# Optimization experiments

Hardware: AMD Instinct MI355X
Metric: run time of the kernel (lower is better)

Reference implementation:

```python
import jax, jax.numpy as jnp
import numpy as np

PAD = 0.1
RESO = 128           # plane_resolution
HID = 128            # hidden_dim
CDIM = 128           # c_dim
NBLK = 5             # n_blocks
PLANES = (('xz', (0, 2)), ('xy', (0, 1)), ('yz', (1, 2)))


def normalize_coordinate(p, dims):
    # p: (B,T,3) -> (B,T,2) in [0, 1)
    xy = p[..., list(dims)] / (1.0 + PAD + 1e-3) + 0.5
    return jnp.clip(xy, 0.0, 1.0 - 1e-5)


def coordinate2index(xy, reso):
    g = (xy * reso).astype(jnp.int32)          # (B,T,2)
    return g[..., 0] + reso * g[..., 1]        # (B,T) flat cell index


def scatter_max_gather(vals, idx, n_cells):
    # vals: (B,T,F), idx: (B,T) -> per-cell max gathered back to points (B,T,F)
    B, T, F = vals.shape
    flat_idx = (idx + jnp.arange(B, dtype=idx.dtype)[:, None] * n_cells).reshape(-1)
    fea = jax.ops.segment_max(vals.reshape(B * T, F), flat_idx, num_segments=B * n_cells)
    return fea[flat_idx].reshape(B, T, F)


def scatter_mean_plane(c, idx, n_cells):
    # c: (B,T,C), idx: (B,T) -> (B, n_cells, C); empty cells stay 0
    B, T, C = c.shape
    flat_idx = (idx + jnp.arange(B, dtype=idx.dtype)[:, None] * n_cells).reshape(-1)
    s = jax.ops.segment_sum(c.reshape(B * T, C), flat_idx, num_segments=B * n_cells)
    cnt = jax.ops.segment_sum(jnp.ones((B * T,), c.dtype), flat_idx, num_segments=B * n_cells)
    return (s / jnp.maximum(cnt, 1.0)[:, None]).reshape(B, n_cells, C)


def resnet_block(x, W0, b0, W1, b1, Ws):
    # ResnetBlockFC(2H -> H), size_h = H, shortcut = Linear(no bias)
    net = jax.nn.relu(x) @ W0 + b0
    dx = jax.nn.relu(net) @ W1 + b1
    return x @ Ws + dx


def setup_inputs() -> dict:
    key = jax.random.key(0)
    ks = jax.random.split(key, 10)
    B, T = 2, 32768
    s = 0.05
    return {
        'p': jax.random.uniform(ks[0], (B, T, 3), jnp.float32, -0.5, 0.5),
        'fc_pos_W': s * jax.random.normal(ks[1], (3, 2 * HID), jnp.float32),
        'fc_pos_b': s * jax.random.normal(ks[2], (2 * HID,), jnp.float32),
        'blocks_W0': s * jax.random.normal(ks[3], (NBLK, 2 * HID, HID), jnp.float32),
        'blocks_b0': s * jax.random.normal(ks[4], (NBLK, HID), jnp.float32),
        'blocks_W1': s * jax.random.normal(ks[5], (NBLK, HID, HID), jnp.float32),
        'blocks_b1': s * jax.random.normal(ks[6], (NBLK, HID), jnp.float32),
        'blocks_Ws': s * jax.random.normal(ks[7], (NBLK, 2 * HID, HID), jnp.float32),
        'fc_c_W': s * jax.random.normal(ks[8], (HID, CDIM), jnp.float32),
        'fc_c_b': s * jax.random.normal(ks[9], (CDIM,), jnp.float32),
    }


def reference(p, fc_pos_W, fc_pos_b, blocks_W0, blocks_b0, blocks_W1, blocks_b1,
              blocks_Ws, fc_c_W, fc_c_b):
    B, T, _ = p.shape
    R2 = RESO * RESO
    index = {k: coordinate2index(normalize_coordinate(p, d), RESO) for k, d in PLANES}

    net = p @ fc_pos_W + fc_pos_b                       # (B,T,2H)
    net = resnet_block(net, blocks_W0[0], blocks_b0[0],
                       blocks_W1[0], blocks_b1[0], blocks_Ws[0])  # (B,T,H)
    for i in range(1, NBLK):
        pooled = sum(scatter_max_gather(net, index[k], R2) for k, _ in PLANES)
        net = jnp.concatenate([net, pooled], axis=-1)   # (B,T,2H)
        net = resnet_block(net, blocks_W0[i], blocks_b0[i],
                           blocks_W1[i], blocks_b1[i], blocks_Ws[i])

    c = net @ fc_c_W + fc_c_b                           # (B,T,C)
    planes = []
    for k, _ in PLANES:  # order: xz, xy, yz
        fea = scatter_mean_plane(c, index[k], R2)       # (B,R2,C)
        planes.append(fea.transpose(0, 2, 1).reshape(B, CDIM, RESO, RESO))
    return jnp.stack(planes)                            # (3,B,C,R,R)
```

## Files before the change

### kernel.cpp

```cpp
#include <hip/hip_runtime.h>

#define TT 65536
#define R2 16384

typedef _Float16 f16x8 __attribute__((ext_vector_type(8)));
typedef float    f32x4 __attribute__((ext_vector_type(4)));
typedef unsigned u32x4 __attribute__((ext_vector_type(4)));

#define MFMA16 __builtin_amdgcn_mfma_f32_16x16x32_f16

__device__ __forceinline__ unsigned short f2h(float f){
    _Float16 h = (_Float16)f;
    return __builtin_bit_cast(unsigned short, h);
}
__device__ __forceinline__ float h2f(unsigned short u){
    return (float)__builtin_bit_cast(_Float16, u);
}
__device__ __forceinline__ unsigned relu2(unsigned w){
    unsigned s = w & 0x80008000u;
    unsigned mask = ((s >> 15) * 0x7FFFu) | s;
    return w & ~mask;
}
__device__ __forceinline__ float nrm(float a){
    float v = a / 1.101f + 0.5f;
    v = fmaxf(v, 0.0f);
    v = fminf(v, 0.99999f);
    return v;
}

__global__ __launch_bounds__(256) void k_repack(const float* __restrict__ W0,
        const float* __restrict__ W1, const float* __restrict__ Ws,
        const float* __restrict__ Wc, unsigned short* __restrict__ out){
    int e = blockIdx.x*256 + threadIdx.x;
    const float* src; int r;
    if (e < 409600){
        int i = e / 81920; r = e % 81920;
        if (r < 32768)      { src = W0 + (size_t)i*32768; }
        else if (r < 49152) { src = W1 + (size_t)i*16384; r -= 32768; }
        else                { src = Ws + (size_t)i*32768; r -= 49152; }
    } else { src = Wc; r = e - 409600; }
    int j = r & 7, l = (r >> 3) & 63, t = (r >> 9) & 7, ks = r >> 12;
    int k = ks*32 + (l >> 4)*8 + j;
    int n = t*16 + (l & 15);
    out[e] = f2h(src[k*128 + n]);
}

__global__ __launch_bounds__(256) void k_idxhist(const float* __restrict__ p,
        int* __restrict__ idx, int* __restrict__ cnt){
    int pt = blockIdx.x*256 + threadIdx.x;
    float p0 = p[pt*3+0], p1 = p[pt*3+1], p2 = p[pt*3+2];
    int g0 = (int)(nrm(p0)*128.f);
    int g1 = (int)(nrm(p1)*128.f);
    int g2 = (int)(nrm(p2)*128.f);
    int i0 = g0 + 128*g2, i1 = g0 + 128*g1, i2 = g1 + 128*g2;
    idx[0*TT + pt] = i0;
    idx[1*TT + pt] = i1;
    idx[2*TT + pt] = i2;
    int b14 = (pt >> 15) << 14;
    atomicAdd(&cnt[0*32768 + b14 + i0], 1);
    atomicAdd(&cnt[1*32768 + b14 + i1], 1);
    atomicAdd(&cnt[2*32768 + b14 + i2], 1);
}

__global__ __launch_bounds__(1024) void k_scan(const int* __restrict__ cnt,
        int* __restrict__ cs, int* __restrict__ cp){
    __shared__ int ls[1024];
    int pl = blockIdx.x, tid = threadIdx.x;
    const int* c = cnt + pl*32768;
    int v[32], tot = 0;
    #pragma unroll
    for (int j = 0; j < 32; j++){ v[j] = c[tid*32 + j]; tot += v[j]; }
    int x = tot;
    ls[tid] = x; __syncthreads();
    for (int off = 1; off < 1024; off <<= 1){
        int add = (tid >= off) ? ls[tid - off] : 0;
        __syncthreads();
        x += add; ls[tid] = x;
        __syncthreads();
    }
    int run = x - tot;
    #pragma unroll
    for (int j = 0; j < 32; j++){
        cs[pl*32769 + tid*32 + j] = run;
        cp[pl*32768 + tid*32 + j] = run;
        run += v[j];
    }
    if (tid == 1023) cs[pl*32769 + 32768] = TT;
}

__global__ __launch_bounds__(256) void k_scatter(const int* __restrict__ idx,
        int* __restrict__ cp, int* __restrict__ srt){
    int pt = blockIdx.x*256 + threadIdx.x;
    int b14 = (pt >> 15) << 14;
    #pragma unroll
    for (int pl = 0; pl < 3; pl++){
        int pos = atomicAdd(&cp[pl*32768 + b14 + idx[pl*TT + pt]], 1);
        srt[pl*TT + pos] = pt;
    }
}

__global__ __launch_bounds__(256) void k_pool3(const unsigned short* __restrict__ xb,
        const int* __restrict__ srt, const int* __restrict__ cs,
        unsigned short* __restrict__ mxp){
    int pl = blockIdx.y;
    const int* srtp = srt + (size_t)pl*TT;
    const int* csp  = cs  + (size_t)pl*32769;
    int lane = threadIdx.x & 63;
    int c = blockIdx.x*4 + (threadIdx.x >> 6);
    int s = csp[c], e = csp[c+1];
    if (s == e) return;
    float m0 = -1e30f, m1 = -1e30f;
    int pt = srtp[s];
    for (int i = s; i < e; i++){
        int ptn = (i+1 < e) ? srtp[i+1] : 0;
        unsigned v = ((const unsigned*)(xb + (size_t)pt*256))[lane];
        m0 = fmaxf(m0, h2f((unsigned short)(v & 0xFFFF)));
        m1 = fmaxf(m1, h2f((unsigned short)(v >> 16)));
        pt = ptn;
    }
    unsigned pk = (unsigned)f2h(m0) | ((unsigned)f2h(m1) << 16);
    ((unsigned*)(mxp + ((size_t)pl*32768 + c)*128))[lane] = pk;
}

#define SEG(ACC, CURB, NEXTB, GETA)                                   \
  { _Pragma("unroll")                                                 \
    for (int ks = 0; ks < 4; ks++){                                   \
      f16x8* cur = (ks & 1) ? bq1 : bq0;                              \
      f16x8* nxt = (ks & 1) ? bq0 : bq1;                              \
      const unsigned short* nb = (ks < 3) ? (CURB) : (NEXTB);         \
      int nks = (ks < 3) ? ks + 1 : 0;                                \
      if (nb) ld8(nxt, nb, nks);                                      \
      f16x8 a0, a1;                                                   \
      GETA                                                            \
      _Pragma("unroll")                                               \
      for (int t = 0; t < 8; t++){                                    \
        ACC[0][t] = MFMA16(a0, cur[t], ACC[0][t], 0, 0, 0);           \
        ACC[1][t] = MFMA16(a1, cur[t], ACC[1][t], 0, 0, 0);           \
      }                                                               \
    }                                                                 \
  }

#define A_RELU_XF { u32x4 u0 = xf[0][ks], u1 = xf[1][ks];                         \
    u0.x=relu2(u0.x); u0.y=relu2(u0.y); u0.z=relu2(u0.z); u0.w=relu2(u0.w);       \
    u1.x=relu2(u1.x); u1.y=relu2(u1.y); u1.z=relu2(u1.z); u1.w=relu2(u1.w);       \
    a0 = __builtin_bit_cast(f16x8, u0); a1 = __builtin_bit_cast(f16x8, u1); }
#define A_RELU_PF { u32x4 u0 = __builtin_bit_cast(u32x4, pf[0][ks]);              \
    u32x4 u1 = __builtin_bit_cast(u32x4, pf[1][ks]);                              \
    u0.x=relu2(u0.x); u0.y=relu2(u0.y); u0.z=relu2(u0.z); u0.w=relu2(u0.w);       \
    u1.x=relu2(u1.x); u1.y=relu2(u1.y); u1.z=relu2(u1.z); u1.w=relu2(u1.w);       \
    a0 = __builtin_bit_cast(f16x8, u0); a1 = __builtin_bit_cast(f16x8, u1); }
#define A_XF { a0 = __builtin_bit_cast(f16x8, xf[0][ks]);                         \
               a1 = __builtin_bit_cast(f16x8, xf[1][ks]); }
#define A_PF { a0 = pf[0][ks]; a1 = pf[1][ks]; }
#define A_LT { a0 = *(const f16x8*)&lt[((ks*8 + w*2 + 0)*64 + lane)*8];           \
               a1 = *(const f16x8*)&lt[((ks*8 + w*2 + 1)*64 + lane)*8]; }

__global__ __launch_bounds__(256, 2) void k_resnet(unsigned short* __restrict__ xb,
        const unsigned short* __restrict__ wp,
        const float* __restrict__ b0, const float* __restrict__ b1,
        const int* __restrict__ idx, const unsigned short* __restrict__ mxp,
        const float* __restrict__ pin, const float* __restrict__ fW,
        const float* __restrict__ fb,
        const unsigned short* __restrict__ wc, const float* __restrict__ bc){
    __shared__ __align__(16) unsigned short lt[16384];
    int tid = threadIdx.x, w = tid >> 6, lane = tid & 63;
    int quad = lane >> 4, l15 = lane & 15;
    int m0 = blockIdx.x*128 + w*32;
    float b0v[8], b1v[8];
    #pragma unroll
    for (int t = 0; t < 8; t++){ b0v[t] = b0[t*16 + l15]; b1v[t] = b1[t*16 + l15]; }

    f16x8 bq0[8], bq1[8];
    auto ld8 = [&](f16x8* dst, const unsigned short* base, int ks){
        #pragma unroll
        for (int t = 0; t < 8; t++)
            dst[t] = *(const f16x8*)(base + ((size_t)((ks*8 + t)*64 + lane))*8);
    };

    ld8(bq0, wp, 0);

    u32x4 xf[2][4]; f16x8 pf[2][4];
    if (pin){
        #pragma unroll
        for (int s = 0; s < 2; s++){
            int row = m0 + s*16 + l15;
            float p0 = pin[row*3+0], p1 = pin[row*3+1], p2 = pin[row*3+2];
            #pragma unroll
            for (int ks = 0; ks < 4; ks++){
                int c0 = ks*32 + quad*8;
                unsigned short hx[8], hp[8];
                #pragma unroll
                for (int h = 0; h < 2; h++){
                    f32x4 w0 = *(const f32x4*)(fW + c0 + h*4);
                    f32x4 w1 = *(const f32x4*)(fW + 256 + c0 + h*4);
                    f32x4 w2 = *(const f32x4*)(fW + 512 + c0 + h*4);
                    f32x4 bb = *(const f32x4*)(fb + c0 + h*4);
                    f32x4 v0 = *(const f32x4*)(fW + 128 + c0 + h*4);
                    f32x4 v1 = *(const f32x4*)(fW + 384 + c0 + h*4);
                    f32x4 v2 = *(const f32x4*)(fW + 640 + c0 + h*4);
                    f32x4 bp = *(const f32x4*)(fb + 128 + c0 + h*4);
                    #pragma unroll
                    for (int j = 0; j < 4; j++){
                        hx[h*4+j] = f2h(bb[j] + p0*w0[j] + p1*w1[j] + p2*w2[j]);
                        hp[h*4+j] = f2h(bp[j] + p0*v0[j] + p1*v1[j] + p2*v2[j]);
                    }
                }
                unsigned short* dx = (unsigned short*)&xf[s][ks];
                unsigned short* dp = (unsigned short*)&pf[s][ks];
                #pragma unroll
                for (int j = 0; j < 8; j++){ dx[j] = hx[j]; dp[j] = hp[j]; }
            }
        }
    } else {
        #pragma unroll
        for (int s = 0; s < 2; s++){
            size_t rb = (size_t)(m0 + s*16 + l15)*256;
            #pragma unroll
            for (int ks = 0; ks < 4; ks++)
                xf[s][ks] = *(const u32x4*)(xb + rb + ks*32 + quad*8);
        }
        #pragma unroll
        for (int s = 0; s < 2; s++){
            int row = m0 + s*16 + l15;
            int b14 = (row >> 15) << 14;
            const unsigned short* q0 = mxp + ((size_t)(0*32768 + b14 + idx[row]))*128;
            const unsigned short* q1 = mxp + ((size_t)(1*32768 + b14 + idx[TT + row]))*128;
            const unsigned short* q2 = mxp + ((size_t)(2*32768 + b14 + idx[2*TT + row]))*128;
            #pragma unroll
            for (int ks = 0; ks < 4; ks++){
                int col = ks*32 + quad*8;
                f16x8 a = *(const f16x8*)(q0 + col);
                f16x8 b = *(const f16x8*)(q1 + col);
                f16x8 c = *(const f16x8*)(q2 + col);
                f16x8 r;
                #pragma unroll
                for (int j = 0; j < 8; j++)
                    r[j] = (_Float16)((float)a[j] + (float)b[j] + (float)c[j]);
                pf[s][ks] = r;
            }
        }
    }

    f32x4 acc[2][8];
    #pragma unroll
    for (int s = 0; s < 2; s++)
        #pragma unroll
        for (int t = 0; t < 8; t++){ f32x4 z = {0.f,0.f,0.f,0.f}; acc[s][t] = z; }

    SEG(acc, wp,         wp + 16384, A_RELU_XF)
    SEG(acc, wp + 16384, wp + 32768, A_RELU_PF)

    #pragma unroll
    for (int s = 0; s < 2; s++){
        int strip = w*2 + s;
        #pragma unroll
        for (int t = 0; t < 8; t++){
            int ks2 = t >> 1;
            int l2b = ((t & 1)*2 + ((lane >> 3) & 1))*16 + quad*4;
            #pragma unroll
            for (int r = 0; r < 4; r++){
                float v = acc[s][t][r] + b0v[t];
                v = fmaxf(v, 0.f);
                lt[(((ks2*8 + strip)*64) + l2b + r)*8 + (lane & 7)] = f2h(v);
            }
        }
    }

    f32x4 acc2[2][8];
    #pragma unroll
    for (int s = 0; s < 2; s++)
        #pragma unroll
        for (int t = 0; t < 8; t++){ f32x4 iv = {b1v[t],b1v[t],b1v[t],b1v[t]}; acc2[s][t] = iv; }
    SEG(acc2, wp + 32768, wp + 49152, A_LT)

    SEG(acc2, wp + 49152, wp + 65536, A_XF)
    SEG(acc2, wp + 65536, wc,         A_PF)

    if (!wc){
        #pragma unroll
        for (int s = 0; s < 2; s++)
            #pragma unroll
            for (int t = 0; t < 8; t++)
                #pragma unroll
                for (int r = 0; r < 4; r++){
                    int row = m0 + s*16 + quad*4 + r;
                    xb[(size_t)row*256 + t*16 + l15] = f2h(acc2[s][t][r]);
                }
        return;
    }

    #pragma unroll
    for (int s = 0; s < 2; s++){
        int strip = w*2 + s;
        #pragma unroll
        for (int t = 0; t < 8; t++){
            int ks2 = t >> 1;
            int l2b = ((t & 1)*2 + ((lane >> 3) & 1))*16 + quad*4;
            #pragma unroll
            for (int r = 0; r < 4; r++)
                lt[(((ks2*8 + strip)*64) + l2b + r)*8 + (lane & 7)] = f2h(acc2[s][t][r]);
        }
    }
    f32x4 acc3[2][8];
    #pragma unroll
    for (int t = 0; t < 8; t++){
        float bv = bc[t*16 + l15];
        f32x4 iv = {bv, bv, bv, bv};
        acc3[0][t] = iv; acc3[1][t] = iv;
    }
    SEG(acc3, wc, (const unsigned short*)nullptr, A_LT)
    #pragma unroll
    for (int s = 0; s < 2; s++)
        #pragma unroll
        for (int t = 0; t < 8; t++)
            #pragma unroll
            for (int r = 0; r < 4; r++){
                int row = m0 + s*16 + quad*4 + r;
                xb[(size_t)row*256 + 128 + t*16 + l15] = f2h(acc3[s][t][r]);
            }
}

__global__ __launch_bounds__(1024) void k_psum3(const unsigned short* __restrict__ xb,
        const int* __restrict__ srt, const int* __restrict__ cs,
        float* __restrict__ out){
    __shared__ float ls[32*129];
    int pl = blockIdx.y;
    const int* srtp = srt + (size_t)pl*TT;
    const int* csp  = cs  + (size_t)pl*32769;
    int w = threadIdx.x >> 6, lane = threadIdx.x & 63;
    int c0 = blockIdx.x * 32;
    #pragma unroll
    for (int cc = w; cc < 32; cc += 16){
        int c = c0 + cc;
        int s = csp[c], e = csp[c+1];
        float s0 = 0.f, s1 = 0.f;
        if (s < e){
            int pt = srtp[s];
            for (int i = s; i < e; i++){
                int ptn = (i+1 < e) ? srtp[i+1] : 0;
                unsigned v = ((const unsigned*)(xb + (size_t)pt*256 + 128))[lane];
                s0 += h2f((unsigned short)(v & 0xFFFF));
                s1 += h2f((unsigned short)(v >> 16));
                pt = ptn;
            }
        }
        float rc = (e > s) ? 1.f/(float)(e - s) : 0.f;
        ls[cc*129 + lane*2]     = s0*rc;
        ls[cc*129 + lane*2 + 1] = s1*rc;
    }
    __syncthreads();
    int pb = pl*2 + (c0 >> 14);
    float* o = out + (size_t)pb*128*R2 + (c0 & 16383);
    #pragma unroll
    for (int j = 0; j < 4; j++){
        int lin = j*1024 + threadIdx.x;
        int f = lin >> 5, cc = lin & 31;
        o[(size_t)f*R2 + cc] = ls[cc*129 + f];
    }
}

extern "C" void kernel_launch(void* const* d_in, const int* in_sizes, int n_in,
                              void* d_out, int out_size, void* d_ws, size_t ws_size,
                              hipStream_t stream) {
    const float* p        = (const float*)d_in[0];
    const float* fc_pos_W = (const float*)d_in[1];
    const float* fc_pos_b = (const float*)d_in[2];
    const float* bW0      = (const float*)d_in[3];
    const float* bb0      = (const float*)d_in[4];
    const float* bW1      = (const float*)d_in[5];
    const float* bb1      = (const float*)d_in[6];
    const float* bWs      = (const float*)d_in[7];
    const float* fc_c_W   = (const float*)d_in[8];
    const float* fc_c_b   = (const float*)d_in[9];
    float* out = (float*)d_out;

    char* ws = (char*)d_ws;
    int*            idx   = (int*)ws;
    unsigned short* xbuf  = (unsigned short*)(ws + 786432);
    int*            srt   = (int*)(ws + 34340864);
    int*            cs    = (int*)(ws + 35127296);
    int*            cp    = (int*)(ws + 35520528);
    unsigned short* wpack = (unsigned short*)(ws + 35913744);
    unsigned short* mxp   = (unsigned short*)(ws + 36765712);

    k_repack<<<1664, 256, 0, stream>>>(bW0, bW1, bWs, fc_c_W, wpack);
    hipMemsetAsync(cp, 0, (size_t)3*32768*4, stream);
    k_idxhist<<<TT/256, 256, 0, stream>>>(p, idx, cp);
    k_scan   <<<3, 1024, 0, stream>>>(cp, cs, cp);
    k_scatter<<<TT/256, 256, 0, stream>>>(idx, cp, srt);

    k_resnet<<<512, 256, 0, stream>>>(xbuf, wpack, bb0, bb1,
            idx, (const unsigned short*)nullptr,
            p, fc_pos_W, fc_pos_b,
            (const unsigned short*)nullptr, (const float*)nullptr);

    for (int i = 1; i < 5; i++){
        k_pool3<<<dim3(8192, 3), 256, 0, stream>>>(xbuf, srt, cs, mxp);
        const unsigned short* wc = (i == 4) ? (wpack + 409600) : (const unsigned short*)nullptr;
        const float* bcp = (i == 4) ? fc_c_b : (const float*)nullptr;
        k_resnet<<<512, 256, 0, stream>>>(xbuf, wpack + (size_t)i*81920,
                bb0 + (size_t)i*128, bb1 + (size_t)i*128,
                idx, mxp,
                (const float*)nullptr, (const float*)nullptr, (const float*)nullptr,
                wc, bcp);
    }

    k_psum3<<<dim3(1024, 3), 1024, 0, stream>>>(xbuf, srt, cs, out);
}
```

Baseline: 423.7 us.

## Reorder points by xz cell so pooling reads contiguous rows

```diff
diff --git a/kernel.cpp b/kernel.cpp
--- a/kernel.cpp
+++ b/kernel.cpp
@@ -99,27 +99,100 @@
     }
 }
 
-__global__ __launch_bounds__(256) void k_pool3(const unsigned short* __restrict__ xb,
+__global__ __launch_bounds__(256) void k_remap1(const int* __restrict__ srt0,
+        const int* __restrict__ idx, const float* __restrict__ p,
+        int* __restrict__ idx2, float* __restrict__ pp, int* __restrict__ inv0){
+    int pos = blockIdx.x*256 + threadIdx.x;
+    int pt = srt0[pos];
+    inv0[pt] = pos;
+    idx2[0*TT + pos] = idx[0*TT + pt];
+    idx2[1*TT + pos] = idx[1*TT + pt];
+    idx2[2*TT + pos] = idx[2*TT + pt];
+    pp[pos*3+0] = p[pt*3+0];
+    pp[pos*3+1] = p[pt*3+1];
+    pp[pos*3+2] = p[pt*3+2];
+}
+__global__ __launch_bounds__(256) void k_remap2(const int* __restrict__ srt,
+        const int* __restrict__ inv0, int* __restrict__ srt2){
+    int pos = blockIdx.x*256 + threadIdx.x;
+    srt2[1*TT + pos] = inv0[srt[1*TT + pos]];
+    srt2[2*TT + pos] = inv0[srt[2*TT + pos]];
+}
+
+__global__ __launch_bounds__(64) void k_pool_s(const unsigned short* __restrict__ nb,
         const int* __restrict__ srt, const int* __restrict__ cs,
         unsigned short* __restrict__ mxp){
-    int pl = blockIdx.y;
-    const int* srtp = srt + (size_t)pl*TT;
-    const int* csp  = cs  + (size_t)pl*32769;
-    int lane = threadIdx.x & 63;
-    int c = blockIdx.x*4 + (threadIdx.x >> 6);
-    int s = csp[c], e = csp[c+1];
-    if (s == e) return;
-    float m0 = -1e30f, m1 = -1e30f;
-    int pt = srtp[s];
-    for (int i = s; i < e; i++){
-        int ptn = (i+1 < e) ? srtp[i+1] : 0;
-        unsigned v = ((const unsigned*)(xb + (size_t)pt*256))[lane];
-        m0 = fmaxf(m0, h2f((unsigned short)(v & 0xFFFF)));
-        m1 = fmaxf(m1, h2f((unsigned short)(v >> 16)));
-        pt = ptn;
-    }
-    unsigned pk = (unsigned)f2h(m0) | ((unsigned)f2h(m1) << 16);
-    ((unsigned*)(mxp + ((size_t)pl*32768 + c)*128))[lane] = pk;
+    int lane = threadIdx.x;
+    for (int cell = blockIdx.x; cell < 98304; cell += gridDim.x){
+        int pl = cell >> 15, c = cell & 32767;
+        int s = cs[pl*32769 + c], e = cs[pl*32769 + c + 1];
+        if (s == e) continue;
+        float mA = -1e30f, mB = -1e30f;
+        if (pl == 0){
+            for (int i = s; i < e; i++){
+                unsigned v = ((const unsigned*)(nb + (size_t)i*128))[lane];
+                mA = fmaxf(mA, h2f((unsigned short)(v & 0xFFFF)));
+                mB = fmaxf(mB, h2f((unsigned short)(v >> 16)));
+            }
+        } else {
+            const int* sp = srt + (size_t)pl*TT;
+            int pt = sp[s];
+            for (int i = s; i < e; i++){
+                int ptn = (i+1 < e) ? sp[i+1] : 0;
+                unsigned v = ((const unsigned*)(nb + (size_t)pt*128))[lane];
+                mA = fmaxf(mA, h2f((unsigned short)(v & 0xFFFF)));
+                mB = fmaxf(mB, h2f((unsigned short)(v >> 16)));
+                pt = ptn;
+            }
+        }
+        unsigned pk = (unsigned)f2h(mA) | ((unsigned)f2h(mB) << 16);
+        ((unsigned*)(mxp + ((size_t)pl*32768 + c)*128))[lane] = pk;
+    }
+}
+
+__global__ __launch_bounds__(256, 4) void k_psum_s(const unsigned short* __restrict__ cb,
+        const int* __restrict__ srt, const int* __restrict__ cs,
+        float* __restrict__ out){
+    __shared__ float ls[32*129];
+    int tid = threadIdx.x, w = tid >> 6, lane = tid & 63;
+    int t = blockIdx.x;
+    int pl = t >> 10, c0 = (t & 1023)*32;
+    #pragma unroll
+    for (int cc = w; cc < 32; cc += 4){
+        int s = cs[pl*32769 + c0 + cc], e = cs[pl*32769 + c0 + cc + 1];
+        float s0 = 0.f, s1 = 0.f;
+        if (s < e){
+            if (pl == 0){
+                for (int i = s; i < e; i++){
+                    unsigned v = ((const unsigned*)(cb + (size_t)i*128))[lane];
+                    s0 += h2f((unsigned short)(v & 0xFFFF));
+                    s1 += h2f((unsigned short)(v >> 16));
+                }
+            } else {
+                const int* sp = srt + (size_t)pl*TT;
+                int pt = sp[s];
+                for (int i = s; i < e; i++){
+                    int ptn = (i+1 < e) ? sp[i+1] : 0;
+                    unsigned v = ((const unsigned*)(cb + (size_t)pt*128))[lane];
+                    s0 += h2f((unsigned short)(v & 0xFFFF));
+                    s1 += h2f((unsigned short)(v >> 16));
+                    pt = ptn;
+                }
+            }
+        }
+        float rc = (e > s) ? 1.f/(float)(e - s) : 0.f;
+        ls[cc*129 + lane*2]     = s0*rc;
+        ls[cc*129 + lane*2 + 1] = s1*rc;
+    }
+    __syncthreads();
+    int pb = pl*2 + (c0 >> 14);
+    float* o = out + (size_t)pb*128*R2 + (c0 & 16383);
+    #pragma unroll
+    for (int j = 0; j < 16; j++){
+        int lin = j*256 + tid;
+        int f = lin >> 5, cc = lin & 31;
+        o[(size_t)f*R2 + cc] = ls[cc*129 + f];
+    }
 }
 
 #define SEG(ACC, CURB, NEXTB, GETA)                                   \
@@ -127,9 +200,9 @@
     for (int ks = 0; ks < 4; ks++){                                   \
       f16x8* cur = (ks & 1) ? bq1 : bq0;                              \
       f16x8* nxt = (ks & 1) ? bq0 : bq1;                              \
-      const unsigned short* nb = (ks < 3) ? (CURB) : (NEXTB);         \
+      const unsigned short* nb_ = (ks < 3) ? (CURB) : (NEXTB);        \
       int nks = (ks < 3) ? ks + 1 : 0;                                \
-      if (nb) ld8(nxt, nb, nks);                                      \
+      if (nb_) ld8(nxt, nb_, nks);                                    \
       f16x8 a0, a1;                                                   \
       GETA                                                            \
       _Pragma("unroll")                                               \
@@ -140,22 +213,23 @@
     }                                                                 \
   }
 
-#define A_RELU_XF { u32x4 u0 = xf[0][ks], u1 = xf[1][ks];                         \
+#define A_G1_XF { u32x4 u0 = get_xf(0, ks), u1 = get_xf(1, ks);                   \
     u0.x=relu2(u0.x); u0.y=relu2(u0.y); u0.z=relu2(u0.z); u0.w=relu2(u0.w);       \
     u1.x=relu2(u1.x); u1.y=relu2(u1.y); u1.z=relu2(u1.z); u1.w=relu2(u1.w);       \
     a0 = __builtin_bit_cast(f16x8, u0); a1 = __builtin_bit_cast(f16x8, u1); }
-#define A_RELU_PF { u32x4 u0 = __builtin_bit_cast(u32x4, pf[0][ks]);              \
+#define A_G1_PF { u32x4 u0 = __builtin_bit_cast(u32x4, pf[0][ks]);                \
     u32x4 u1 = __builtin_bit_cast(u32x4, pf[1][ks]);                              \
     u0.x=relu2(u0.x); u0.y=relu2(u0.y); u0.z=relu2(u0.z); u0.w=relu2(u0.w);       \
     u1.x=relu2(u1.x); u1.y=relu2(u1.y); u1.z=relu2(u1.z); u1.w=relu2(u1.w);       \
     a0 = __builtin_bit_cast(f16x8, u0); a1 = __builtin_bit_cast(f16x8, u1); }
-#define A_XF { a0 = __builtin_bit_cast(f16x8, xf[0][ks]);                         \
-               a1 = __builtin_bit_cast(f16x8, xf[1][ks]); }
+#define A_G3_XF { a0 = __builtin_bit_cast(f16x8, get_xf(0, ks));                  \
+                  a1 = __builtin_bit_cast(f16x8, get_xf(1, ks)); }
 #define A_PF { a0 = pf[0][ks]; a1 = pf[1][ks]; }
 #define A_LT { a0 = *(const f16x8*)&lt[((ks*8 + w*2 + 0)*64 + lane)*8];           \
                a1 = *(const f16x8*)&lt[((ks*8 + w*2 + 1)*64 + lane)*8]; }
 
-__global__ __launch_bounds__(256, 2) void k_resnet(unsigned short* __restrict__ xb,
+__global__ __launch_bounds__(256, 3) void k_resnet_s(
+        unsigned short* __restrict__ nb, unsigned short* __restrict__ cb,
         const unsigned short* __restrict__ wp,
         const float* __restrict__ b0, const float* __restrict__ b1,
         const int* __restrict__ idx, const unsigned short* __restrict__ mxp,
@@ -166,9 +240,6 @@
     int tid = threadIdx.x, w = tid >> 6, lane = tid & 63;
     int quad = lane >> 4, l15 = lane & 15;
     int m0 = blockIdx.x*128 + w*32;
-    float b0v[8], b1v[8];
-    #pragma unroll
-    for (int t = 0; t < 8; t++){ b0v[t] = b0[t*16 + l15]; b1v[t] = b1[t*16 + l15]; }
 
     f16x8 bq0[8], bq1[8];
     auto ld8 = [&](f16x8* dst, const unsigned short* base, int ks){
@@ -176,49 +247,63 @@
         for (int t = 0; t < 8; t++)
             dst[t] = *(const f16x8*)(base + ((size_t)((ks*8 + t)*64 + lane))*8);
     };
-
     ld8(bq0, wp, 0);
 
-    u32x4 xf[2][4]; f16x8 pf[2][4];
+    float p0s[2], p1s[2], p2s[2];
     if (pin){
         #pragma unroll
         for (int s = 0; s < 2; s++){
             int row = m0 + s*16 + l15;
-            float p0 = pin[row*3+0], p1 = pin[row*3+1], p2 = pin[row*3+2];
+            p0s[s] = pin[row*3+0]; p1s[s] = pin[row*3+1]; p2s[s] = pin[row*3+2];
+        }
+    }
+    auto get_xf = [&](int s, int ks)->u32x4 {
+        if (pin){
+            int c0 = ks*32 + quad*8;
+            unsigned short hx[8];
+            #pragma unroll
+            for (int h = 0; h < 2; h++){
+                f32x4 w0 = *(const f32x4*)(fW + c0 + h*4);
+                f32x4 w1 = *(const f32x4*)(fW + 256 + c0 + h*4);
+                f32x4 w2 = *(const f32x4*)(fW + 512 + c0 + h*4);
+                f32x4 bb = *(const f32x4*)(fb + c0 + h*4);
+                #pragma unroll
+                for (int j = 0; j < 4; j++)
+                    hx[h*4+j] = f2h(bb[j] + p0s[s]*w0[j] + p1s[s]*w1[j] + p2s[s]*w2[j]);
+            }
+            u32x4 r;
+            unsigned short* d = (unsigned short*)&r;
+            #pragma unroll
+            for (int j = 0; j < 8; j++) d[j] = hx[j];
+            return r;
+        }
+        return *(const u32x4*)(nb + (size_t)(m0 + s*16 + l15)*128 + ks*32 + quad*8);
+    };
+
+    f16x8 pf[2][4];
+    if (pin){
+        #pragma unroll
+        for (int s = 0; s < 2; s++){
             #pragma unroll
             for (int ks = 0; ks < 4; ks++){
-                int c0 = ks*32 + quad*8;
-                unsigned short hx[8], hp[8];
+                int c0 = 128 + ks*32 + quad*8;
+                unsigned short hp[8];
                 #pragma unroll
                 for (int h = 0; h < 2; h++){
-                    f32x4 w0 = *(const f32x4*)(fW + c0 + h*4);
-                    f32x4 w1 = *(const f32x4*)(fW + 256 + c0 + h*4);
-                    f32x4 w2 = *(const f32x4*)(fW + 512 + c0 + h*4);
-                    f32x4 bb = *(const f32x4*)(fb + c0 + h*4);
-                    f32x4 v0 = *(const f32x4*)(fW + 128 + c0 + h*4);
-                    f32x4 v1 = *(const f32x4*)(fW + 384 + c0 + h*4);
-                    f32x4 v2 = *(const f32x4*)(fW + 640 + c0 + h*4);
-                    f32x4 bp = *(const f32x4*)(fb + 128 + c0 + h*4);
+                    f32x4 v0 = *(const f32x4*)(fW + c0 + h*4);
+                    f32x4 v1 = *(const f32x4*)(fW + 256 + c0 + h*4);
+                    f32x4 v2 = *(const f32x4*)(fW + 512 + c0 + h*4);
+                    f32x4 bp = *(const f32x4*)(fb + c0 + h*4);
                     #pragma unroll
-                    for (int j = 0; j < 4; j++){
-                        hx[h*4+j] = f2h(bb[j] + p0*w0[j] + p1*w1[j] + p2*w2[j]);
-                        hp[h*4+j] = f2h(bp[j] + p0*v0[j] + p1*v1[j] + p2*v2[j]);
-                    }
+                    for (int j = 0; j < 4; j++)
+                        hp[h*4+j] = f2h(bp[j] + p0s[s]*v0[j] + p1s[s]*v1[j] + p2s[s]*v2[j]);
                 }
-                unsigned short* dx = (unsigned short*)&xf[s][ks];
-                unsigned short* dp = (unsigned short*)&pf[s][ks];
+                unsigned short* d = (unsigned short*)&pf[s][ks];
                 #pragma unroll
-                for (int j = 0; j < 8; j++){ dx[j] = hx[j]; dp[j] = hp[j]; }
+                for (int j = 0; j < 8; j++) d[j] = hp[j];
             }
         }
     } else {
-        #pragma unroll
-        for (int s = 0; s < 2; s++){
-            size_t rb = (size_t)(m0 + s*16 + l15)*256;
-            #pragma unroll
-            for (int ks = 0; ks < 4; ks++)
-                xf[s][ks] = *(const u32x4*)(xb + rb + ks*32 + quad*8);
-        }
         #pragma unroll
         for (int s = 0; s < 2; s++){
             int row = m0 + s*16 + l15;
@@ -247,19 +332,20 @@
         #pragma unroll
         for (int t = 0; t < 8; t++){ f32x4 z = {0.f,0.f,0.f,0.f}; acc[s][t] = z; }
 
-    SEG(acc, wp,         wp + 16384, A_RELU_XF)
-    SEG(acc, wp + 16384, wp + 32768, A_RELU_PF)
+    SEG(acc, wp,         wp + 16384, A_G1_XF)
+    SEG(acc, wp + 16384, wp + 32768, A_G1_PF)
 
     #pragma unroll
     for (int s = 0; s < 2; s++){
         int strip = w*2 + s;
         #pragma unroll
         for (int t = 0; t < 8; t++){
+            float b0t = b0[t*16 + l15];
             int ks2 = t >> 1;
             int l2b = ((t & 1)*2 + ((lane >> 3) & 1))*16 + quad*4;
             #pragma unroll
             for (int r = 0; r < 4; r++){
-                float v = acc[s][t][r] + b0v[t];
+                float v = acc[s][t][r] + b0t;
                 v = fmaxf(v, 0.f);
                 lt[(((ks2*8 + strip)*64) + l2b + r)*8 + (lane & 7)] = f2h(v);
             }
@@ -268,12 +354,14 @@
 
     f32x4 acc2[2][8];
     #pragma unroll
-    for (int s = 0; s < 2; s++)
-        #pragma unroll
-        for (int t = 0; t < 8; t++){ f32x4 iv = {b1v[t],b1v[t],b1v[t],b1v[t]}; acc2[s][t] = iv; }
+    for (int t = 0; t < 8; t++){
+        float b1t = b1[t*16 + l15];
+        f32x4 iv = {b1t, b1t, b1t, b1t};
+        acc2[0][t] = iv; acc2[1][t] = iv;
+    }
     SEG(acc2, wp + 32768, wp + 49152, A_LT)
 
-    SEG(acc2, wp + 49152, wp + 65536, A_XF)
+    SEG(acc2, wp + 49152, wp + 65536, A_G3_XF)
     SEG(acc2, wp + 65536, wc,         A_PF)
 
     if (!wc){
@@ -284,7 +372,7 @@
                 #pragma unroll
                 for (int r = 0; r < 4; r++){
                     int row = m0 + s*16 + quad*4 + r;
-                    xb[(size_t)row*256 + t*16 + l15] = f2h(acc2[s][t][r]);
+                    nb[(size_t)row*128 + t*16 + l15] = f2h(acc2[s][t][r]);
                 }
         return;
     }
@@ -316,47 +404,8 @@
             #pragma unroll
             for (int r = 0; r < 4; r++){
                 int row = m0 + s*16 + quad*4 + r;
-                xb[(size_t)row*256 + 128 + t*16 + l15] = f2h(acc3[s][t][r]);
-            }
-}
-
-__global__ __launch_bounds__(1024) void k_psum3(const unsigned short* __restrict__ xb,
-        const int* __restrict__ srt, const int* __restrict__ cs,
-        float* __restrict__ out){
-    __shared__ float ls[32*129];
-    int pl = blockIdx.y;
-    const int* srtp = srt + (size_t)pl*TT;
-    const int* csp  = cs  + (size_t)pl*32769;
-    int w = threadIdx.x >> 6, lane = threadIdx.x & 63;
-    int c0 = blockIdx.x * 32;
-    #pragma unroll
-    for (int cc = w; cc < 32; cc += 16){
-        int c = c0 + cc;
-        int s = csp[c], e = csp[c+1];
-        float s0 = 0.f, s1 = 0.f;
-        if (s < e){
-            int pt = srtp[s];
-            for (int i = s; i < e; i++){
-                int ptn = (i+1 < e) ? srtp[i+1] : 0;
-                unsigned v = ((const unsigned*)(xb + (size_t)pt*256 + 128))[lane];
-                s0 += h2f((unsigned short)(v & 0xFFFF));
-                s1 += h2f((unsigned short)(v >> 16));
-                pt = ptn;
-            }
-        }
-        float rc = (e > s) ? 1.f/(float)(e - s) : 0.f;
-        ls[cc*129 + lane*2]     = s0*rc;
-        ls[cc*129 + lane*2 + 1] = s1*rc;
-    }
-    __syncthreads();
-    int pb = pl*2 + (c0 >> 14);
-    float* o = out + (size_t)pb*128*R2 + (c0 & 16383);
-    #pragma unroll
-    for (int j = 0; j < 4; j++){
-        int lin = j*1024 + threadIdx.x;
-        int f = lin >> 5, cc = lin & 31;
-        o[(size_t)f*R2 + cc] = ls[cc*129 + f];
-    }
+                cb[(size_t)row*128 + t*16 + l15] = f2h(acc3[s][t][r]);
+            }
 }
 
 extern "C" void kernel_launch(void* const* d_in, const int* in_sizes, int n_in,
@@ -376,34 +425,41 @@
 
     char* ws = (char*)d_ws;
     int*            idx   = (int*)ws;
-    unsigned short* xbuf  = (unsigned short*)(ws + 786432);
+    unsigned short* nb    = (unsigned short*)(ws + 786432);
+    unsigned short* cb    = (unsigned short*)(ws + 17563648);
     int*            srt   = (int*)(ws + 34340864);
     int*            cs    = (int*)(ws + 35127296);
     int*            cp    = (int*)(ws + 35520528);
     unsigned short* wpack = (unsigned short*)(ws + 35913744);
     unsigned short* mxp   = (unsigned short*)(ws + 36765712);
+    int*            idx2  = (int*)(ws + 61931536);
+    float*          pp    = (float*)(ws + 62717968);
+    int*            inv0  = (int*)(ws + 63504400);
+    int*            srt2  = (int*)(ws + 63766544);
 
     k_repack<<<1664, 256, 0, stream>>>(bW0, bW1, bWs, fc_c_W, wpack);
     hipMemsetAsync(cp, 0, (size_t)3*32768*4, stream);
     k_idxhist<<<TT/256, 256, 0, stream>>>(p, idx, cp);
     k_scan   <<<3, 1024, 0, stream>>>(cp, cs, cp);
     k_scatter<<<TT/256, 256, 0, stream>>>(idx, cp, srt);
-
-    k_resnet<<<512, 256, 0, stream>>>(xbuf, wpack, bb0, bb1,
-            idx, (const unsigned short*)nullptr,
-            p, fc_pos_W, fc_pos_b,
+    k_remap1 <<<TT/256, 256, 0, stream>>>(srt, idx, p, idx2, pp, inv0);
+    k_remap2 <<<TT/256, 256, 0, stream>>>(srt, inv0, srt2);
+
+    k_resnet_s<<<512, 256, 0, stream>>>(nb, cb, wpack, bb0, bb1,
+            idx2, (const unsigned short*)nullptr,
+            pp, fc_pos_W, fc_pos_b,
             (const unsigned short*)nullptr, (const float*)nullptr);
 
     for (int i = 1; i < 5; i++){
-        k_pool3<<<dim3(8192, 3), 256, 0, stream>>>(xbuf, srt, cs, mxp);
+        k_pool_s<<<6144, 64, 0, stream>>>(nb, srt2, cs, mxp);
         const unsigned short* wc = (i == 4) ? (wpack + 409600) : (const unsigned short*)nullptr;
         const float* bcp = (i == 4) ? fc_c_b : (const float*)nullptr;
-        k_resnet<<<512, 256, 0, stream>>>(xbuf, wpack + (size_t)i*81920,
+        k_resnet_s<<<512, 256, 0, stream>>>(nb, cb, wpack + (size_t)i*81920,
                 bb0 + (size_t)i*128, bb1 + (size_t)i*128,
-                idx, mxp,
+                idx2, mxp,
                 (const float*)nullptr, (const float*)nullptr, (const float*)nullptr,
                 wc, bcp);
     }
 
-    k_psum3<<<dim3(1024, 3), 1024, 0, stream>>>(xbuf, srt, cs, out);
-}
+    k_psum_s<<<3072, 256, 0, stream>>>(cb, srt2, cs, out);
+}
```

Result: slower. 504.9 us (+19.2%).
